# Optimization experiments

Hardware: AMD Instinct MI355X
Metric: run time of the kernel (lower is better)

## Reference

```python
import jax, jax.numpy as jnp
import numpy as np

N_NODES = 50000
N_EDGES = 800000
N_LABEL_EDGES = 200000
IN_CH = 256
HID = 64
OUT_CH = 64


def gcn_conv(x, W, b, edge_index, n_nodes):
    """PyG GCNConv: symmetric-normalized aggregation with self-loops.
    out[col] = sum_row norm(row,col) * (x @ W)[row] + b
    """
    xw = x @ W  # [N, out]
    loops = jnp.arange(n_nodes, dtype=edge_index.dtype)
    row = jnp.concatenate([edge_index[0], loops])  # source
    col = jnp.concatenate([edge_index[1], loops])  # target
    deg = jax.ops.segment_sum(jnp.ones_like(col, dtype=xw.dtype), col, num_segments=n_nodes)
    dis = jnp.where(deg > 0, jax.lax.rsqrt(deg), 0.0)
    norm = dis[row] * dis[col]  # [E+N]
    out = jax.ops.segment_sum(xw[row] * norm[:, None], col, num_segments=n_nodes)
    return out + b


def setup_inputs() -> dict:
    key = jax.random.key(0)
    k0, k1, k2, k3, k4 = jax.random.split(key, 5)
    x = jax.random.normal(k0, (N_NODES, IN_CH), dtype=jnp.float32)
    edge_index = jax.random.randint(k1, (2, N_EDGES), 0, N_NODES, dtype=jnp.int32)
    edge_label_index = jax.random.randint(k2, (2, N_LABEL_EDGES), 0, N_NODES, dtype=jnp.int32)
    W1 = jax.random.normal(k3, (IN_CH, HID), dtype=jnp.float32) * (1.0 / np.sqrt(IN_CH))
    b1 = jnp.zeros((HID,), dtype=jnp.float32)
    W2 = jax.random.normal(k4, (HID, OUT_CH), dtype=jnp.float32) * (1.0 / np.sqrt(HID))
    b2 = jnp.zeros((OUT_CH,), dtype=jnp.float32)
    return {"x": x, "edge_index": edge_index, "edge_label_index": edge_label_index,
            "W1": W1, "b1": b1, "W2": W2, "b2": b2}


def reference(x, edge_index, edge_label_index, W1, b1, W2, b2):
    n = x.shape[0]
    # encode: two GCNConv layers with ReLU between
    h = jax.nn.relu(gcn_conv(x, W1, b1, edge_index, n))
    z = gcn_conv(h, W2, b2, edge_index, n)
    # decode: gather node pairs, elementwise multiply, sum over features
    src, dst = edge_label_index[0], edge_label_index[1]
    return jnp.sum(z[src] * z[dst], axis=1)  # [N_LABEL_EDGES]
```

## Files before the change

### kernel.cpp

```cpp
#include <hip/hip_runtime.h>
#include <hip/hip_bf16.h>


constexpr int NC = 512;
constexpr int NBPAD = 256;
constexpr int BSHIFT = 8;

__device__ __forceinline__ unsigned short f2bf(float f) {
    unsigned u = __float_as_uint(f);
    return (unsigned short)((u + 0x7FFF + ((u >> 16) & 1)) >> 16);
}
__device__ __forceinline__ float bf2f(unsigned short h) {
    return __uint_as_float(((unsigned)h) << 16);
}
__device__ __forceinline__ float4 bf4_to_f4(ushort4 u) {
    return make_float4(bf2f(u.x), bf2f(u.y), bf2f(u.z), bf2f(u.w));
}

__global__ __launch_bounds__(256) void hist_kernel(const int* __restrict__ col,
                                                   int* __restrict__ histCM,
                                                   int* __restrict__ bsums, int E, int CE) {
    __shared__ int hl[NBPAD];
    const int t = threadIdx.x, c = blockIdx.x;
    hl[t] = 0;
    __syncthreads();
    const int s = c * CE, e = min(E, s + CE);
    for (int i = s + t; i < e; i += 256) atomicAdd(&hl[col[i] >> BSHIFT], 1);
    __syncthreads();
    const int v = hl[t];
    histCM[c * NBPAD + t] = v;
    if (v) atomicAdd(&bsums[t], v);
}

__global__ __launch_bounds__(256) void rowscan_kernel(const int* __restrict__ histCM,
                                                      const int* __restrict__ bsums,
                                                      int* __restrict__ offsBM) {
    __shared__ int red[256];
    __shared__ int sc[256];
    const int t = threadIdx.x, b = blockIdx.x;
    red[t] = (t < b) ? bsums[t] : 0;
    __syncthreads();
    for (int off = 128; off > 0; off >>= 1) {
        if (t < off) red[t] += red[t + off];
        __syncthreads();
    }
    const int base = red[0];
    const int a0 = histCM[(2 * t) * NBPAD + b];
    const int a1 = histCM[(2 * t + 1) * NBPAD + b];
    const int ps = a0 + a1;
    sc[t] = ps;
    __syncthreads();
    for (int off = 1; off < 256; off <<= 1) {
        int u = (t >= off) ? sc[t - off] : 0;
        __syncthreads();
        sc[t] += u;
        __syncthreads();
    }
    const int excl = sc[t] - ps;
    offsBM[b * NC + 2 * t] = base + excl;
    offsBM[b * NC + 2 * t + 1] = base + excl + a0;
}

__global__ __launch_bounds__(256) void reorder_kernel(const int* __restrict__ row,
                                                      const int* __restrict__ col,
                                                      const int* __restrict__ offsBM,
                                                      int2* __restrict__ part, int E, int CE) {
    __shared__ int cur[NBPAD];
    const int t = threadIdx.x, c = blockIdx.x;
    cur[t] = offsBM[t * NC + c];
    __syncthreads();
    const int s = c * CE, e = min(E, s + CE);
    for (int i = s + t; i < e; i += 256) {
        const int r = row[i], cl = col[i];
        const int p = atomicAdd(&cur[cl >> BSHIFT], 1);
        part[p] = make_int2(r, cl);
    }
}

__global__ __launch_bounds__(256) void bucket_csr_kernel(const int2* __restrict__ part,
                                                         const int* __restrict__ offsBM,
                                                         int* __restrict__ csr,
                                                         int* __restrict__ offs,
                                                         float* __restrict__ dis,
                                                         int N, int E, int nbk) {
    __shared__ int cnt[256];
    __shared__ int sc[256];
    const int t = threadIdx.x, b = blockIdx.x;
    const int base = b << BSHIFT;
    const int bstart = offsBM[b * NC];
    const int bend = (b + 1 < NBPAD) ? offsBM[(b + 1) * NC] : E;
    const int m = bend - bstart;
    cnt[t] = 0;
    __syncthreads();
    for (int i = t; i < m; i += 256) atomicAdd(&cnt[part[bstart + i].y - base], 1);
    __syncthreads();
    const int v = cnt[t];
    sc[t] = v;
    __syncthreads();
    for (int off = 1; off < 256; off <<= 1) {
        int u = (t >= off) ? sc[t - off] : 0;
        __syncthreads();
        sc[t] += u;
        __syncthreads();
    }
    const int excl = sc[t] - v;
    const int node = base + t;
    if (node < N) {
        offs[node] = bstart + excl;
        dis[node] = rsqrtf((float)(v + 1));
    }
    sc[t] = excl;
    __syncthreads();
    for (int i = t; i < m; i += 256) {
        const int2 ec = part[bstart + i];
        const int p = atomicAdd(&sc[ec.y - base], 1);
        csr[bstart + p] = ec.x;
    }
    if (b == nbk - 1 && t == 0) offs[N] = E;
}

template <int K>
__global__ __launch_bounds__(256) void gemm_tile(const float* __restrict__ X,
                                                 const float* __restrict__ W,
                                                 const float* __restrict__ rowscale,
                                                 unsigned short* __restrict__ Y, int nrows) {
    __shared__ float sX[64 * 64];
    __shared__ float sW[64 * 64];
    const int tid = threadIdx.x;
    const int tx = tid & 15;
    const int ty = tid >> 4;
    const int rowbase = blockIdx.x * 64;

    float acc[16];
    #pragma unroll
    for (int i = 0; i < 16; ++i) acc[i] = 0.f;

    const int lr = tid & 63;
    const int lq = tid >> 6;
    int grow = rowbase + lr;
    if (grow >= nrows) grow = nrows - 1;
    const float* xrow = X + (long)grow * K;

    for (int kc = 0; kc < K; kc += 64) {
        if (kc) __syncthreads();
        #pragma unroll
        for (int i = 0; i < 4; ++i) {
            const int o = tid * 4 + i * 1024;
            *(float4*)&sW[o] = *(const float4*)&W[(long)kc * 64 + o];
        }
        #pragma unroll
        for (int t = 0; t < 4; ++t) {
            const int k = lq * 16 + t * 4;
            const float4 v = *(const float4*)&xrow[kc + k];
            sX[(k + 0) * 64 + lr] = v.x;
            sX[(k + 1) * 64 + lr] = v.y;
            sX[(k + 2) * 64 + lr] = v.z;
            sX[(k + 3) * 64 + lr] = v.w;
        }
        __syncthreads();
        #pragma unroll 4
        for (int k = 0; k < 64; ++k) {
            const float4 xv = *(const float4*)&sX[k * 64 + ty * 4];
            const float4 wv = *(const float4*)&sW[k * 64 + tx * 4];
            acc[0]  = fmaf(xv.x, wv.x, acc[0]);
            acc[1]  = fmaf(xv.x, wv.y, acc[1]);
            acc[2]  = fmaf(xv.x, wv.z, acc[2]);
            acc[3]  = fmaf(xv.x, wv.w, acc[3]);
            acc[4]  = fmaf(xv.y, wv.x, acc[4]);
            acc[5]  = fmaf(xv.y, wv.y, acc[5]);
            acc[6]  = fmaf(xv.y, wv.z, acc[6]);
            acc[7]  = fmaf(xv.y, wv.w, acc[7]);
            acc[8]  = fmaf(xv.z, wv.x, acc[8]);
            acc[9]  = fmaf(xv.z, wv.y, acc[9]);
            acc[10] = fmaf(xv.z, wv.z, acc[10]);
            acc[11] = fmaf(xv.z, wv.w, acc[11]);
            acc[12] = fmaf(xv.w, wv.x, acc[12]);
            acc[13] = fmaf(xv.w, wv.y, acc[13]);
            acc[14] = fmaf(xv.w, wv.z, acc[14]);
            acc[15] = fmaf(xv.w, wv.w, acc[15]);
        }
    }

    #pragma unroll
    for (int i = 0; i < 4; ++i) {
        const int orow = rowbase + ty * 4 + i;
        if (orow < nrows) {
            const float d = rowscale[orow];
            ushort4 ov;
            ov.x = f2bf(d * acc[i * 4 + 0]);
            ov.y = f2bf(d * acc[i * 4 + 1]);
            ov.z = f2bf(d * acc[i * 4 + 2]);
            ov.w = f2bf(d * acc[i * 4 + 3]);
            *(ushort4*)&Y[(long)orow * 64 + tx * 4] = ov;
        }
    }
}

template <bool RELU, bool OUT_BF16>
__global__ __launch_bounds__(256) void agg_kernel(const unsigned short* __restrict__ xs,
                                                  const int* __restrict__ csr,
                                                  const int* __restrict__ offs,
                                                  const float* __restrict__ dis,
                                                  const float* __restrict__ bias,
                                                  void* __restrict__ out, int n) {
    __shared__ int sidx[4][64];
    const int wv = threadIdx.x >> 6;
    const int lane = threadIdx.x & 63;
    const int grp = lane >> 4;
    const int fl = lane & 15;
    const int i = blockIdx.x * 4 + wv;
    if (i >= n) return;
    float4 acc = make_float4(0.f, 0.f, 0.f, 0.f);
    if (grp == 0)
        acc = bf4_to_f4(*(const ushort4*)&xs[(long)i * 64 + fl * 4]);
    const int s = offs[i];
    const int e = offs[i + 1];
    for (int jb = s; jb < e; jb += 64) {
        const int nb = min(64, e - jb);
        if (lane < nb) sidx[wv][lane] = csr[jb + lane];
        int u = grp;
        for (; u + 4 < nb; u += 8) {
            const int r0 = sidx[wv][u];
            const int r1 = sidx[wv][u + 4];
            const float4 v0 = bf4_to_f4(*(const ushort4*)&xs[(long)r0 * 64 + fl * 4]);
            const float4 v1 = bf4_to_f4(*(const ushort4*)&xs[(long)r1 * 64 + fl * 4]);
            acc.x += v0.x + v1.x; acc.y += v0.y + v1.y;
            acc.z += v0.z + v1.z; acc.w += v0.w + v1.w;
        }
        for (; u < nb; u += 4) {
            const int r0 = sidx[wv][u];
            const float4 v0 = bf4_to_f4(*(const ushort4*)&xs[(long)r0 * 64 + fl * 4]);
            acc.x += v0.x; acc.y += v0.y; acc.z += v0.z; acc.w += v0.w;
        }
    }
    acc.x += __shfl_xor(acc.x, 16); acc.y += __shfl_xor(acc.y, 16);
    acc.z += __shfl_xor(acc.z, 16); acc.w += __shfl_xor(acc.w, 16);
    acc.x += __shfl_xor(acc.x, 32); acc.y += __shfl_xor(acc.y, 32);
    acc.z += __shfl_xor(acc.z, 32); acc.w += __shfl_xor(acc.w, 32);
    if (grp == 0) {
        const float di = dis[i];
        const float4 b = *(const float4*)&bias[fl * 4];
        float4 o;
        o.x = fmaf(acc.x, di, b.x); o.y = fmaf(acc.y, di, b.y);
        o.z = fmaf(acc.z, di, b.z); o.w = fmaf(acc.w, di, b.w);
        if (RELU) {
            o.x = fmaxf(o.x, 0.f); o.y = fmaxf(o.y, 0.f);
            o.z = fmaxf(o.z, 0.f); o.w = fmaxf(o.w, 0.f);
        }
        if (OUT_BF16) {
            ushort4 ov;
            ov.x = f2bf(o.x); ov.y = f2bf(o.y); ov.z = f2bf(o.z); ov.w = f2bf(o.w);
            *(ushort4*)&((unsigned short*)out)[(long)i * 64 + fl * 4] = ov;
        } else {
            *(float4*)&((float*)out)[(long)i * 64 + fl * 4] = o;
        }
    }
}

__global__ __launch_bounds__(256) void decode_kernel(const unsigned short* __restrict__ z,
                                                     const int* __restrict__ src,
                                                     const int* __restrict__ dst,
                                                     float* __restrict__ out, int L) {
    const int t = blockIdx.x * 256 + threadIdx.x;
    const int e = t >> 4;
    const int fl = t & 15;
    if (e >= L) return;
    const int s = src[e];
    const int d = dst[e];
    const float4 a = bf4_to_f4(*(const ushort4*)&z[(long)s * 64 + fl * 4]);
    const float4 b = bf4_to_f4(*(const ushort4*)&z[(long)d * 64 + fl * 4]);
    float p = a.x * b.x + a.y * b.y + a.z * b.z + a.w * b.w;
    p += __shfl_xor(p, 8); p += __shfl_xor(p, 4);
    p += __shfl_xor(p, 2); p += __shfl_xor(p, 1);
    if (fl == 0) out[e] = p;
}

extern "C" void kernel_launch(void* const* d_in, const int* in_sizes, int n_in,
                              void* d_out, int out_size, void* d_ws, size_t ws_size,
                              hipStream_t stream) {
    const float* x   = (const float*)d_in[0];
    const int*   ei  = (const int*)d_in[1];
    const int*   eli = (const int*)d_in[2];
    const float* W1  = (const float*)d_in[3];
    const float* b1  = (const float*)d_in[4];
    const float* W2  = (const float*)d_in[5];
    const float* b2  = (const float*)d_in[6];
    float* out = (float*)d_out;

    const int N = in_sizes[0] / 256;
    const int E = in_sizes[1] / 2;
    const int L = in_sizes[2] / 2;
    const int* row = ei;
    const int* col = ei + E;
    const int* src = eli;
    const int* dst = eli + L;

    char* w = (char*)d_ws;
    unsigned short* xs = (unsigned short*)w;  w += (size_t)N * 64 * 2;
    float* h   = (float*)w;  w += (size_t)N * 64 * 4;
    unsigned short* z = (unsigned short*)w;  w += (size_t)N * 64 * 2;
    int*   csr = (int*)w;    w += (size_t)E * 4;
    int*   offs = (int*)w;   w += (size_t)(N + 1) * 4;
    float* dis = (float*)w;  w += (size_t)N * 4;
    int2*  part = (int2*)w;  w += (size_t)E * 8;
    int* histCM = (int*)w;   w += (size_t)NC * NBPAD * 4;
    int* offsBM = (int*)w;   w += (size_t)NBPAD * NC * 4;
    int* bsums  = (int*)w;   w += NBPAD * 4;

    const int CE = (E + NC - 1) / NC;
    const int nbk = (N + (1 << BSHIFT) - 1) >> BSHIFT;

    hipMemsetAsync(bsums, 0, NBPAD * sizeof(int), stream);
    hist_kernel<<<NC, 256, 0, stream>>>(col, histCM, bsums, E, CE);
    rowscan_kernel<<<NBPAD, 256, 0, stream>>>(histCM, bsums, offsBM);
    reorder_kernel<<<NC, 256, 0, stream>>>(row, col, offsBM, part, E, CE);
    bucket_csr_kernel<<<nbk, 256, 0, stream>>>(part, offsBM, csr, offs, dis, N, E, nbk);

    gemm_tile<256><<<(N + 63) / 64, 256, 0, stream>>>(x, W1, dis, xs, N);
    agg_kernel<true, false><<<(N + 3) / 4, 256, 0, stream>>>(xs, csr, offs, dis, b1, h, N);
    gemm_tile<64><<<(N + 63) / 64, 256, 0, stream>>>(h, W2, dis, xs, N);
    agg_kernel<false, true><<<(N + 3) / 4, 256, 0, stream>>>(xs, csr, offs, dis, b2, z, N);
    decode_kernel<<<(L + 15) / 16, 256, 0, stream>>>(z, src, dst, out, L);
}
```

Baseline: 235.1 us.

## Pack partition entries into one int and assign 16 lanes per node in aggregation

The partition buffer now stores each edge as one 32-bit word (source shifted left by 8, OR the low 8 bits of the target), halving that buffer's traffic in the reorder and bucket-CSR kernels. The aggregation kernel drops the shared-memory index staging and the 4-way split within a wavefront. It now gives each node a 16-lane group that walks its neighbour list directly, unrolled by four, so no cross-group shuffle reduction is needed. The packing assumes node ids below 2^23, and per-lane divergence from varying degrees within a wavefront may reduce efficiency.

```diff
diff --git a/kernel.cpp b/kernel.cpp
--- a/kernel.cpp
+++ b/kernel.cpp
@@ -64,7 +64,7 @@
 __global__ __launch_bounds__(256) void reorder_kernel(const int* __restrict__ row,
                                                       const int* __restrict__ col,
                                                       const int* __restrict__ offsBM,
-                                                      int2* __restrict__ part, int E, int CE) {
+                                                      int* __restrict__ part, int E, int CE) {
     __shared__ int cur[NBPAD];
     const int t = threadIdx.x, c = blockIdx.x;
     cur[t] = offsBM[t * NC + c];
@@ -73,11 +73,11 @@
     for (int i = s + t; i < e; i += 256) {
         const int r = row[i], cl = col[i];
         const int p = atomicAdd(&cur[cl >> BSHIFT], 1);
-        part[p] = make_int2(r, cl);
-    }
-}
-
-__global__ __launch_bounds__(256) void bucket_csr_kernel(const int2* __restrict__ part,
+        part[p] = (r << 8) | (cl & 255);
+    }
+}
+
+__global__ __launch_bounds__(256) void bucket_csr_kernel(const int* __restrict__ part,
                                                          const int* __restrict__ offsBM,
                                                          int* __restrict__ csr,
                                                          int* __restrict__ offs,
@@ -92,7 +92,7 @@
     const int m = bend - bstart;
     cnt[t] = 0;
     __syncthreads();
-    for (int i = t; i < m; i += 256) atomicAdd(&cnt[part[bstart + i].y - base], 1);
+    for (int i = t; i < m; i += 256) atomicAdd(&cnt[part[bstart + i] & 255], 1);
     __syncthreads();
     const int v = cnt[t];
     sc[t] = v;
@@ -112,9 +112,9 @@
     sc[t] = excl;
     __syncthreads();
     for (int i = t; i < m; i += 256) {
-        const int2 ec = part[bstart + i];
-        const int p = atomicAdd(&sc[ec.y - base], 1);
-        csr[bstart + p] = ec.x;
+        const int pc = part[bstart + i];
+        const int p = atomicAdd(&sc[pc & 255], 1);
+        csr[bstart + p] = pc >> 8;
     }
     if (b == nbk - 1 && t == 0) offs[N] = E;
 }
@@ -203,57 +203,46 @@
                                                   const float* __restrict__ dis,
                                                   const float* __restrict__ bias,
                                                   void* __restrict__ out, int n) {
-    __shared__ int sidx[4][64];
-    const int wv = threadIdx.x >> 6;
-    const int lane = threadIdx.x & 63;
-    const int grp = lane >> 4;
-    const int fl = lane & 15;
-    const int i = blockIdx.x * 4 + wv;
+    const int t = threadIdx.x;
+    const int fl = t & 15;
+    const int i = blockIdx.x * 16 + (t >> 4);
     if (i >= n) return;
-    float4 acc = make_float4(0.f, 0.f, 0.f, 0.f);
-    if (grp == 0)
-        acc = bf4_to_f4(*(const ushort4*)&xs[(long)i * 64 + fl * 4]);
+    float4 acc = bf4_to_f4(*(const ushort4*)&xs[(long)i * 64 + fl * 4]);
     const int s = offs[i];
     const int e = offs[i + 1];
-    for (int jb = s; jb < e; jb += 64) {
-        const int nb = min(64, e - jb);
-        if (lane < nb) sidx[wv][lane] = csr[jb + lane];
-        int u = grp;
-        for (; u + 4 < nb; u += 8) {
-            const int r0 = sidx[wv][u];
-            const int r1 = sidx[wv][u + 4];
-            const float4 v0 = bf4_to_f4(*(const ushort4*)&xs[(long)r0 * 64 + fl * 4]);
-            const float4 v1 = bf4_to_f4(*(const ushort4*)&xs[(long)r1 * 64 + fl * 4]);
-            acc.x += v0.x + v1.x; acc.y += v0.y + v1.y;
-            acc.z += v0.z + v1.z; acc.w += v0.w + v1.w;
-        }
-        for (; u < nb; u += 4) {
-            const int r0 = sidx[wv][u];
-            const float4 v0 = bf4_to_f4(*(const ushort4*)&xs[(long)r0 * 64 + fl * 4]);
-            acc.x += v0.x; acc.y += v0.y; acc.z += v0.z; acc.w += v0.w;
-        }
-    }
-    acc.x += __shfl_xor(acc.x, 16); acc.y += __shfl_xor(acc.y, 16);
-    acc.z += __shfl_xor(acc.z, 16); acc.w += __shfl_xor(acc.w, 16);
-    acc.x += __shfl_xor(acc.x, 32); acc.y += __shfl_xor(acc.y, 32);
-    acc.z += __shfl_xor(acc.z, 32); acc.w += __shfl_xor(acc.w, 32);
-    if (grp == 0) {
-        const float di = dis[i];
-        const float4 b = *(const float4*)&bias[fl * 4];
-        float4 o;
-        o.x = fmaf(acc.x, di, b.x); o.y = fmaf(acc.y, di, b.y);
-        o.z = fmaf(acc.z, di, b.z); o.w = fmaf(acc.w, di, b.w);
-        if (RELU) {
-            o.x = fmaxf(o.x, 0.f); o.y = fmaxf(o.y, 0.f);
-            o.z = fmaxf(o.z, 0.f); o.w = fmaxf(o.w, 0.f);
-        }
-        if (OUT_BF16) {
-            ushort4 ov;
-            ov.x = f2bf(o.x); ov.y = f2bf(o.y); ov.z = f2bf(o.z); ov.w = f2bf(o.w);
-            *(ushort4*)&((unsigned short*)out)[(long)i * 64 + fl * 4] = ov;
-        } else {
-            *(float4*)&((float*)out)[(long)i * 64 + fl * 4] = o;
-        }
+    int j = s;
+    for (; j + 3 < e; j += 4) {
+        const int r0 = csr[j],     r1 = csr[j + 1];
+        const int r2 = csr[j + 2], r3 = csr[j + 3];
+        const float4 v0 = bf4_to_f4(*(const ushort4*)&xs[(long)r0 * 64 + fl * 4]);
+        const float4 v1 = bf4_to_f4(*(const ushort4*)&xs[(long)r1 * 64 + fl * 4]);
+        const float4 v2 = bf4_to_f4(*(const ushort4*)&xs[(long)r2 * 64 + fl * 4]);
+        const float4 v3 = bf4_to_f4(*(const ushort4*)&xs[(long)r3 * 64 + fl * 4]);
+        acc.x += (v0.x + v1.x) + (v2.x + v3.x);
+        acc.y += (v0.y + v1.y) + (v2.y + v3.y);
+        acc.z += (v0.z + v1.z) + (v2.z + v3.z);
+        acc.w += (v0.w + v1.w) + (v2.w + v3.w);
+    }
+    for (; j < e; ++j) {
+        const int r0 = csr[j];
+        const float4 v0 = bf4_to_f4(*(const ushort4*)&xs[(long)r0 * 64 + fl * 4]);
+        acc.x += v0.x; acc.y += v0.y; acc.z += v0.z; acc.w += v0.w;
+    }
+    const float di = dis[i];
+    const float4 b = *(const float4*)&bias[fl * 4];
+    float4 o;
+    o.x = fmaf(acc.x, di, b.x); o.y = fmaf(acc.y, di, b.y);
+    o.z = fmaf(acc.z, di, b.z); o.w = fmaf(acc.w, di, b.w);
+    if (RELU) {
+        o.x = fmaxf(o.x, 0.f); o.y = fmaxf(o.y, 0.f);
+        o.z = fmaxf(o.z, 0.f); o.w = fmaxf(o.w, 0.f);
+    }
+    if (OUT_BF16) {
+        ushort4 ov;
+        ov.x = f2bf(o.x); ov.y = f2bf(o.y); ov.z = f2bf(o.z); ov.w = f2bf(o.w);
+        *(ushort4*)&((unsigned short*)out)[(long)i * 64 + fl * 4] = ov;
+    } else {
+        *(float4*)&((float*)out)[(long)i * 64 + fl * 4] = o;
     }
 }
 
@@ -302,7 +291,7 @@
     int*   csr = (int*)w;    w += (size_t)E * 4;
     int*   offs = (int*)w;   w += (size_t)(N + 1) * 4;
     float* dis = (float*)w;  w += (size_t)N * 4;
-    int2*  part = (int2*)w;  w += (size_t)E * 8;
+    int*   part = (int*)w;   w += (size_t)E * 4;
     int* histCM = (int*)w;   w += (size_t)NC * NBPAD * 4;
     int* offsBM = (int*)w;   w += (size_t)NBPAD * NC * 4;
     int* bsums  = (int*)w;   w += NBPAD * 4;
@@ -317,8 +306,8 @@
     bucket_csr_kernel<<<nbk, 256, 0, stream>>>(part, offsBM, csr, offs, dis, N, E, nbk);
 
     gemm_tile<256><<<(N + 63) / 64, 256, 0, stream>>>(x, W1, dis, xs, N);
-    agg_kernel<true, false><<<(N + 3) / 4, 256, 0, stream>>>(xs, csr, offs, dis, b1, h, N);
+    agg_kernel<true, false><<<(N + 15) / 16, 256, 0, stream>>>(xs, csr, offs, dis, b1, h, N);
     gemm_tile<64><<<(N + 63) / 64, 256, 0, stream>>>(h, W2, dis, xs, N);
-    agg_kernel<false, true><<<(N + 3) / 4, 256, 0, stream>>>(xs, csr, offs, dis, b2, z, N);
+    agg_kernel<false, true><<<(N + 15) / 16, 256, 0, stream>>>(xs, csr, offs, dis, b2, z, N);
     decode_kernel<<<(L + 15) / 16, 256, 0, stream>>>(z, src, dst, out, L);
 }
```

Result: faster. 224.9 us (-4.3%).
